# Kernel optimization log

Hardware: AMD Instinct MI355X
Metric: run time of the kernel (lower is better)

Reference implementation:

```python
import jax, jax.numpy as jnp
import numpy as np

K = [3072, 1024, 512, 256, 128, 64, 32, 16, 8, 4, 2, 1]
R = 2          # Repeats
B = 8192       # batch
LEAK = 0.01    # LeakyReLU negative_slope
EP, EM, E0V = 50.0, -70.0, -65.0  # synapse reversal potentials


def setup_inputs() -> dict:
    key = jax.random.key(0)
    ks = jax.random.split(key, 40)
    std = float(np.sqrt(2.0 / K[0]))  # torch init: normal std sqrt(2/in_features)
    inp = {"x": jax.random.normal(ks[0], (B, K[0]), jnp.float32)}
    for j, name in enumerate(["ap1", "ap2", "am1", "am2", "g0"]):
        inp[name] = jax.random.normal(ks[1 + j], (R, K[0]), jnp.float32) * std
    for i in range(len(K) - 1):
        f = K[i] // K[i + 1]
        inp[f"w{i}"] = jax.random.normal(ks[6 + i], (R, K[i + 1], f), jnp.float32) * float(np.sqrt(1.0 / f))
        inp[f"b{i}"] = jnp.zeros((R, K[i + 1]), jnp.float32)  # bias.data.zero_()
    inp["root_w"] = jax.random.normal(ks[30], (1, R), jnp.float32) * 0.5
    inp["root_b"] = jnp.zeros((1,), jnp.float32)
    return inp


def _synapse(x, ap1, ap2, am1, am2, g0):
    # x: [B, N]; params: [R, N] -> out: [R, B, N]
    def g(a1, a2):
        return jnp.exp(jnp.clip(a1[:, None, :] * x[None, :, :] + a2[:, None, :], -60.0, 60.0))
    gp = g(ap1, ap2)
    gm = g(am1, am2)
    gz = g0[:, None, :]
    return (gp * EP + gm * EM + gz * E0V) / (gp + gm + gz)


def _tree(y, Ws, Bs):
    # y: [R, B, K0]; tree-structured (kronecker) linear layers + leaky relu
    for i in range(len(K) - 1):
        f = K[i] // K[i + 1]
        y = y.reshape(R, -1, K[i + 1], f)          # group fan-in children
        y = jnp.einsum('rbnf,rnf->rbn', y, Ws[i]) + Bs[i][:, None, :]
        y = jnp.where(y >= 0, y, LEAK * y)          # LeakyReLU(0.01)
    return y  # [R, B, 1]


def reference(x, ap1, ap2, am1, am2, g0,
              w0, w1, w2, w3, w4, w5, w6, w7, w8, w9, w10,
              b0, b1, b2, b3, b4, b5, b6, b7, b8, b9, b10,
              root_w, root_b):
    Ws = [w0, w1, w2, w3, w4, w5, w6, w7, w8, w9, w10]
    Bs = [b0, b1, b2, b3, b4, b5, b6, b7, b8, b9, b10]
    y = _synapse(x, ap1, ap2, am1, am2, g0)  # [R, B, 3072]
    y = _tree(y, Ws, Bs)                     # [R, B, 1]
    feats = y[:, :, 0].T                     # [B, R] (concat of repeat outputs)
    return feats @ root_w.T + root_b         # root linear -> [B, 1]
```

## Files before the change

kernel.cpp:

```cpp
#include <hip/hip_runtime.h>

#define K0 3072
#define BPB 16
#define BLOCK 1024

struct KtreeArgs {
  const float* x;
  const float* ap1; const float* ap2; const float* am1; const float* am2; const float* g0;
  const float* w[11];
  const float* bs[11];
  const float* root_w; const float* root_b;
  float* out;
};

__device__ __forceinline__ float lrelu(float v) {
  return v >= 0.0f ? v : 0.01f * v;
}

__global__ __launch_bounds__(BLOCK, 4) void ktree_synapse_kernel(KtreeArgs A) {
  const int tid = threadIdx.x;
  const int wv  = tid >> 6;
  const int l   = tid & 63;
  const int c   = wv & 7;
  const int r   = wv >> 3;

  const int node512 = c * 64 + l;
  const int kb      = node512 * 6;

  const int o_syn = r * K0 + kb;
  const float* p_ap1 = A.ap1 + o_syn;
  const float* p_ap2 = A.ap2 + o_syn;
  const float* p_am1 = A.am1 + o_syn;
  const float* p_am2 = A.am2 + o_syn;
  const float* p_g0  = A.g0  + o_syn;

  float w0v[6], b0a, b0b;
  {
    const int o = (r * 1024 + 2 * node512) * 3;
    #pragma unroll
    for (int j = 0; j < 6; ++j) w0v[j] = A.w[0][o + j];
    b0a = A.bs[0][r * 1024 + 2 * node512];
    b0b = A.bs[0][r * 1024 + 2 * node512 + 1];
  }
  float w1a, w1b, b1v;
  {
    const int n = r * 512 + node512;
    w1a = A.w[1][n * 2 + 0];
    w1b = A.w[1][n * 2 + 1];
    b1v = A.bs[1][n];
  }
  float wso[6], wst[6], bsv[6];
  #pragma unroll
  for (int s = 0; s < 6; ++s) {
    const int mo  = c * (32 >> s) + (l >> (s + 1));
    const int idx = r * (256 >> s) + mo;
    const int odd = (l >> s) & 1;
    wso[s] = A.w[2 + s][idx * 2 + odd];
    wst[s] = A.w[2 + s][idx * 2 + (odd ^ 1)];
    bsv[s] = A.bs[2 + s][idx];
  }

  __shared__ float lds_buf[BPB][2][8];
  const int bbase = blockIdx.x * BPB;

  for (int bi = 0; bi < BPB; ++bi) {
    const int b = bbase + bi;
    const float2* xp = reinterpret_cast<const float2*>(A.x + (size_t)b * K0 + kb);
    const float2 xa = xp[0], xb = xp[1], xc = xp[2];
    const float xv[6] = {xa.x, xa.y, xb.x, xb.y, xc.x, xc.y};

    float acc0 = b0a, acc1 = b0b;
    #pragma unroll
    for (int j = 0; j < 6; ++j) {
      float tp = fmaf(p_ap1[j], xv[j], p_ap2[j]);
      float tm = fmaf(p_am1[j], xv[j], p_am2[j]);
      tp = fminf(fmaxf(tp, -60.0f), 60.0f);
      tm = fminf(fmaxf(tm, -60.0f), 60.0f);
      const float gp = __expf(tp);
      const float gm = __expf(tm);
      const float gz = p_g0[j];
      const float num = fmaf(50.0f, gp, fmaf(-70.0f, gm, -65.0f * gz));
      const float den = gp + gm + gz;
      const float s = num * __builtin_amdgcn_rcpf(den);
      if (j < 3) acc0 = fmaf(w0v[j], s, acc0);
      else       acc1 = fmaf(w0v[j], s, acc1);
    }
    acc0 = lrelu(acc0);
    acc1 = lrelu(acc1);
    float v = lrelu(fmaf(w1a, acc0, fmaf(w1b, acc1, b1v)));

    #pragma unroll
    for (int s = 0; s < 6; ++s) {
      const float u = __shfl_xor(v, 1 << s, 64);
      v = lrelu(fmaf(wso[s], v, fmaf(wst[s], u, bsv[s])));
    }
    if (l == 0) lds_buf[bi][r][c] = v;
  }
  __syncthreads();

  if (tid < BPB) {
    const int b = bbase + tid;
    float o = A.root_b[0];
    #pragma unroll
    for (int rr = 0; rr < 2; ++rr) {
      float v8[8];
      #pragma unroll
      for (int q = 0; q < 8; ++q) v8[q] = lds_buf[tid][rr][q];
      float v4[4];
      #pragma unroll
      for (int n = 0; n < 4; ++n)
        v4[n] = lrelu(fmaf(A.w[8][(rr * 4 + n) * 2 + 0], v8[2 * n],
                      fmaf(A.w[8][(rr * 4 + n) * 2 + 1], v8[2 * n + 1],
                           A.bs[8][rr * 4 + n])));
      float v2[2];
      #pragma unroll
      for (int n = 0; n < 2; ++n)
        v2[n] = lrelu(fmaf(A.w[9][(rr * 2 + n) * 2 + 0], v4[2 * n],
                      fmaf(A.w[9][(rr * 2 + n) * 2 + 1], v4[2 * n + 1],
                           A.bs[9][rr * 2 + n])));
      const float v1 = lrelu(fmaf(A.w[10][rr * 2 + 0], v2[0],
                             fmaf(A.w[10][rr * 2 + 1], v2[1],
                                  A.bs[10][rr])));
      o = fmaf(A.root_w[rr], v1, o);
    }
    A.out[b] = o;
  }
}

extern "C" void kernel_launch(void* const* d_in, const int* in_sizes, int n_in,
                              void* d_out, int out_size, void* d_ws, size_t ws_size,
                              hipStream_t stream) {
  KtreeArgs A;
  A.x   = (const float*)d_in[0];
  A.ap1 = (const float*)d_in[1];
  A.ap2 = (const float*)d_in[2];
  A.am1 = (const float*)d_in[3];
  A.am2 = (const float*)d_in[4];
  A.g0  = (const float*)d_in[5];
  for (int i = 0; i < 11; ++i) {
    A.w[i]  = (const float*)d_in[6 + 2 * i];
    A.bs[i] = (const float*)d_in[7 + 2 * i];
  }
  A.root_w = (const float*)d_in[28];
  A.root_b = (const float*)d_in[29];
  A.out = (float*)d_out;

  const int grid = 8192 / BPB;
  hipLaunchKernelGGL(ktree_synapse_kernel, dim3(grid), dim3(BLOCK), 0, stream, A);
}
```

Baseline: 216.5 us.

## Split tree kernel into chunked phase1 over row tiles plus small phase2 reduction

The single fused kernel is split into two launches. The first assigns each block one of 8 column chunks and a 32-row tile, with 4 waves per repeat processing rows in parallel. It keeps synapse parameters in registers and writes per-row, per-chunk partial results to a workspace buffer. A second small kernel reads those 16 values per row and evaluates the top tree levels and the root linear layer. This gives more, smaller blocks and more row-level parallelism per block, removing the serial 16-row loop, at the cost of an extra launch and a global round trip through the workspace.

```diff
diff --git a/kernel.cpp b/kernel.cpp
--- a/kernel.cpp
+++ b/kernel.cpp
@@ -1,8 +1,10 @@
 #include <hip/hip_runtime.h>
 
 #define K0 3072
-#define BPB 16
-#define BLOCK 1024
+#define NCHUNK 8
+#define RPB 32
+#define BLOCK1 512
+#define ROWWAVES 4
 
 struct KtreeArgs {
   const float* x;
@@ -17,23 +19,31 @@
   return v >= 0.0f ? v : 0.01f * v;
 }
 
-__global__ __launch_bounds__(BLOCK, 4) void ktree_synapse_kernel(KtreeArgs A) {
+__global__ __launch_bounds__(BLOCK1, 2) void ktree_phase1(KtreeArgs A, float* wsb) {
   const int tid = threadIdx.x;
   const int wv  = tid >> 6;
   const int l   = tid & 63;
-  const int c   = wv & 7;
-  const int r   = wv >> 3;
+  const int r   = wv >> 2;
+  const int rs  = wv & 3;
+  const int c     = blockIdx.x & (NCHUNK - 1);
+  const int btile = blockIdx.x >> 3;
+  const int bbase = btile * RPB;
 
   const int node512 = c * 64 + l;
   const int kb      = node512 * 6;
 
-  const int o_syn = r * K0 + kb;
-  const float* p_ap1 = A.ap1 + o_syn;
-  const float* p_ap2 = A.ap2 + o_syn;
-  const float* p_am1 = A.am1 + o_syn;
-  const float* p_am2 = A.am2 + o_syn;
-  const float* p_g0  = A.g0  + o_syn;
-
+  float p1[6], p2[6], m1[6], m2[6], z0[6];
+  {
+    const int o = r * K0 + kb;
+    #pragma unroll
+    for (int j = 0; j < 6; ++j) {
+      p1[j] = A.ap1[o + j];
+      p2[j] = A.ap2[o + j];
+      m1[j] = A.am1[o + j];
+      m2[j] = A.am2[o + j];
+      z0[j] = A.g0[o + j];
+    }
+  }
   float w0v[6], b0a, b0b;
   {
     const int o = (r * 1024 + 2 * node512) * 3;
@@ -49,7 +59,7 @@
     w1b = A.w[1][n * 2 + 1];
     b1v = A.bs[1][n];
   }
-  float wso[6], wst[6], bsv[6];
+  float wso[6], wst[6], bsw[6];
   #pragma unroll
   for (int s = 0; s < 6; ++s) {
     const int mo  = c * (32 >> s) + (l >> (s + 1));
@@ -57,28 +67,26 @@
     const int odd = (l >> s) & 1;
     wso[s] = A.w[2 + s][idx * 2 + odd];
     wst[s] = A.w[2 + s][idx * 2 + (odd ^ 1)];
-    bsv[s] = A.bs[2 + s][idx];
+    bsw[s] = A.bs[2 + s][idx];
   }
 
-  __shared__ float lds_buf[BPB][2][8];
-  const int bbase = blockIdx.x * BPB;
-
-  for (int bi = 0; bi < BPB; ++bi) {
-    const int b = bbase + bi;
-    const float2* xp = reinterpret_cast<const float2*>(A.x + (size_t)b * K0 + kb);
+  #pragma unroll
+  for (int i = 0; i < RPB / ROWWAVES; ++i) {
+    const int row = bbase + rs + ROWWAVES * i;
+    const float2* xp = reinterpret_cast<const float2*>(A.x + (size_t)row * K0 + kb);
     const float2 xa = xp[0], xb = xp[1], xc = xp[2];
     const float xv[6] = {xa.x, xa.y, xb.x, xb.y, xc.x, xc.y};
 
     float acc0 = b0a, acc1 = b0b;
     #pragma unroll
     for (int j = 0; j < 6; ++j) {
-      float tp = fmaf(p_ap1[j], xv[j], p_ap2[j]);
-      float tm = fmaf(p_am1[j], xv[j], p_am2[j]);
+      float tp = fmaf(p1[j], xv[j], p2[j]);
+      float tm = fmaf(m1[j], xv[j], m2[j]);
       tp = fminf(fmaxf(tp, -60.0f), 60.0f);
       tm = fminf(fmaxf(tm, -60.0f), 60.0f);
       const float gp = __expf(tp);
       const float gm = __expf(tm);
-      const float gz = p_g0[j];
+      const float gz = z0[j];
       const float num = fmaf(50.0f, gp, fmaf(-70.0f, gm, -65.0f * gz));
       const float den = gp + gm + gz;
       const float s = num * __builtin_amdgcn_rcpf(den);
@@ -92,39 +100,52 @@
     #pragma unroll
     for (int s = 0; s < 6; ++s) {
       const float u = __shfl_xor(v, 1 << s, 64);
-      v = lrelu(fmaf(wso[s], v, fmaf(wst[s], u, bsv[s])));
+      v = lrelu(fmaf(wso[s], v, fmaf(wst[s], u, bsw[s])));
     }
-    if (l == 0) lds_buf[bi][r][c] = v;
+    if (l == 0) wsb[row * 16 + r * 8 + c] = v;
   }
-  __syncthreads();
+}
 
-  if (tid < BPB) {
-    const int b = bbase + tid;
-    float o = A.root_b[0];
+__global__ __launch_bounds__(256) void ktree_phase2(const float* __restrict__ wsb,
+                                                    const float* __restrict__ w8,
+                                                    const float* __restrict__ b8,
+                                                    const float* __restrict__ w9,
+                                                    const float* __restrict__ b9,
+                                                    const float* __restrict__ w10,
+                                                    const float* __restrict__ b10,
+                                                    const float* __restrict__ root_w,
+                                                    const float* __restrict__ root_b,
+                                                    float* __restrict__ out) {
+  const int b = blockIdx.x * blockDim.x + threadIdx.x;
+  const float4* wp = reinterpret_cast<const float4*>(wsb + b * 16);
+  float v8[16];
+  #pragma unroll
+  for (int q = 0; q < 4; ++q) {
+    const float4 t = wp[q];
+    v8[4 * q + 0] = t.x; v8[4 * q + 1] = t.y; v8[4 * q + 2] = t.z; v8[4 * q + 3] = t.w;
+  }
+  float o = root_b[0];
+  #pragma unroll
+  for (int rr = 0; rr < 2; ++rr) {
+    const float* v = v8 + rr * 8;
+    float v4[4];
     #pragma unroll
-    for (int rr = 0; rr < 2; ++rr) {
-      float v8[8];
-      #pragma unroll
-      for (int q = 0; q < 8; ++q) v8[q] = lds_buf[tid][rr][q];
-      float v4[4];
-      #pragma unroll
-      for (int n = 0; n < 4; ++n)
-        v4[n] = lrelu(fmaf(A.w[8][(rr * 4 + n) * 2 + 0], v8[2 * n],
-                      fmaf(A.w[8][(rr * 4 + n) * 2 + 1], v8[2 * n + 1],
-                           A.bs[8][rr * 4 + n])));
-      float v2[2];
-      #pragma unroll
-      for (int n = 0; n < 2; ++n)
-        v2[n] = lrelu(fmaf(A.w[9][(rr * 2 + n) * 2 + 0], v4[2 * n],
-                      fmaf(A.w[9][(rr * 2 + n) * 2 + 1], v4[2 * n + 1],
-                           A.bs[9][rr * 2 + n])));
-      const float v1 = lrelu(fmaf(A.w[10][rr * 2 + 0], v2[0],
-                             fmaf(A.w[10][rr * 2 + 1], v2[1],
-                                  A.bs[10][rr])));
-      o = fmaf(A.root_w[rr], v1, o);
-    }
-    A.out[b] = o;
+    for (int n = 0; n < 4; ++n)
+      v4[n] = lrelu(fmaf(w8[(rr * 4 + n) * 2 + 0], v[2 * n],
+                    fmaf(w8[(rr * 4 + n) * 2 + 1], v[2 * n + 1],
+                         b8[rr * 4 + n])));
+    float v2[2];
+    #pragma unroll
+    for (int n = 0; n < 2; ++n)
+      v2[n] = lrelu(fmaf(w9[(rr * 2 + n) * 2 + 0], v4[2 * n],
+                    fmaf(w9[(rr * 2 + n) * 2 + 1], v4[2 * n + 1],
+                         b9[rr * 2 + n])));
+    const float v1 = lrelu(fmaf(w10[rr * 2 + 0], v2[0],
+                           fmaf(w10[rr * 2 + 1], v2[1],
+                                b10[rr])));
+    o = fmaf(root_w[rr], v1, o);
   }
+  out[b] = o;
 }
 
 extern "C" void kernel_launch(void* const* d_in, const int* in_sizes, int n_in,
@@ -145,6 +166,11 @@
   A.root_b = (const float*)d_in[29];
   A.out = (float*)d_out;
 
-  const int grid = 8192 / BPB;
-  hipLaunchKernelGGL(ktree_synapse_kernel, dim3(grid), dim3(BLOCK), 0, stream, A);
+  float* wsb = (float*)d_ws;
+  const int grid1 = NCHUNK * (8192 / RPB);
+  hipLaunchKernelGGL(ktree_phase1, dim3(grid1), dim3(BLOCK1), 0, stream, A, wsb);
+
+  hipLaunchKernelGGL(ktree_phase2, dim3(8192 / 256), dim3(256), 0, stream,
+                     wsb, A.w[8], A.bs[8], A.w[9], A.bs[9], A.w[10], A.bs[10],
+                     A.root_w, A.root_b, A.out);
 }
```

After: 221.5 us. +2.3%, slower.
